# Kernel optimization log

Hardware: AMD Instinct MI355X
Metric: run time of the kernel (lower is better)

The kernel has to match this reference:

```python
import jax, jax.numpy as jnp
import numpy as np

N = 10000
E = 160000
B = 16
NEG_SLOPE = 0.2


def gat_conv(x, src, dst, W, a_src, a_dst, b, heads, ch):
    # x: [N, F_in]; src/dst: [E'] (self-loops included); W: [F_in, heads*ch]
    n = x.shape[0]
    h = (x @ W).reshape(n, heads, ch)                     # [N,H,C]
    alpha_src = jnp.sum(h * a_src, axis=-1)               # [N,H]
    alpha_dst = jnp.sum(h * a_dst, axis=-1)               # [N,H]
    e = jax.nn.leaky_relu(alpha_src[src] + alpha_dst[dst], NEG_SLOPE)  # [E,H]
    # segment softmax over edges grouped by destination node
    m = jax.ops.segment_max(e, dst, num_segments=n)       # [N,H]
    ex = jnp.exp(e - m[dst])                              # [E,H]
    denom = jax.ops.segment_sum(ex, dst, num_segments=n)  # [N,H]
    alpha = ex / denom[dst]                               # [E,H]
    out = jax.ops.segment_sum(alpha[:, :, None] * h[src], dst, num_segments=n)  # [N,H,C]
    return out.reshape(n, heads * ch) + b


def setup_inputs() -> dict:
    key = jax.random.key(0)
    ks = jax.random.split(key, 16)
    glorot = lambda k, shp: jax.random.normal(k, shp, jnp.float32) * np.sqrt(2.0 / (shp[0] + shp[-1]))
    inp = {
        "x": jax.random.normal(ks[0], (N, 128), jnp.float32),
        "edge_index": jax.random.randint(ks[1], (2, E), 0, N, jnp.int64),
        "batch": jnp.sort(jax.random.randint(ks[2], (N,), 0, B, jnp.int64)),
        # conv1: 128 -> 128 per head, 8 heads
        "W1": glorot(ks[3], (128, 8 * 128)),
        "att_src1": glorot(ks[4], (8, 128)),
        "att_dst1": glorot(ks[5], (8, 128)),
        "b1": jnp.zeros((8 * 128,), jnp.float32),
        # conv2: 1024 -> 64 per head, 8 heads
        "W2": glorot(ks[6], (1024, 8 * 64)),
        "att_src2": glorot(ks[7], (8, 64)),
        "att_dst2": glorot(ks[8], (8, 64)),
        "b2": jnp.zeros((8 * 64,), jnp.float32),
        "fc1_w": glorot(ks[9], (512, 32)),
        "fc1_b": jnp.zeros((32,), jnp.float32),
        "fc2_w": glorot(ks[10], (32, 10)),
        "fc2_b": jnp.zeros((10,), jnp.float32),
    }
    return inp


def reference(x, edge_index, batch, W1, att_src1, att_dst1, b1,
              W2, att_src2, att_dst2, b2, fc1_w, fc1_b, fc2_w, fc2_b):
    n = x.shape[0]
    loop = jnp.arange(n, dtype=edge_index.dtype)
    src = jnp.concatenate([edge_index[0], loop])  # PyG add_self_loops=True
    dst = jnp.concatenate([edge_index[1], loop])
    h = jax.nn.elu(gat_conv(x, src, dst, W1, att_src1, att_dst1, b1, 8, 128))   # [N,1024]
    h = jax.nn.elu(gat_conv(h, src, dst, W2, att_src2, att_dst2, b2, 8, 64))    # [N,512]
    # global mean pool over graphs
    sums = jax.ops.segment_sum(h, batch, num_segments=B)                        # [B,512]
    cnt = jax.ops.segment_sum(jnp.ones((n,), h.dtype), batch, num_segments=B)
    g = sums / jnp.maximum(cnt, 1.0)[:, None]
    g = jax.nn.elu(g @ fc1_w + fc1_b)
    return g @ fc2_w + fc2_b                                                    # [B,10]
```

## Files before the change

### kernel.cpp

```cpp
#include <hip/hip_runtime.h>
#include <math.h>

#define HEADS 8
#define NEG 0.2f

typedef unsigned short ushort_t;
typedef __attribute__((ext_vector_type(8))) short short8;
typedef float f32x4 __attribute__((ext_vector_type(4)));

__device__ inline ushort_t f2bf(float f) {
  union { float f; unsigned u; } v; v.f = f;
  unsigned r = (v.u + 0x7FFF + ((v.u >> 16) & 1)) >> 16;
  return (ushort_t)r;
}

__device__ inline float4 bf4(uint2 v) {
  union { unsigned u; float f; } a, b, c, d;
  a.u = v.x << 16; b.u = v.x & 0xffff0000u;
  c.u = v.y << 16; d.u = v.y & 0xffff0000u;
  return make_float4(a.f, b.f, c.f, d.f);
}

__global__ void zero_k(int* __restrict__ p, int n) {
  int i = blockIdx.x * blockDim.x + threadIdx.x;
  int stride = gridDim.x * blockDim.x;
  for (; i < n; i += stride) p[i] = 0;
}

__global__ void prep_k(const int* __restrict__ ei, int* __restrict__ src,
                       int* __restrict__ dst, int* __restrict__ deg, int E, int Nn) {
  int i = blockIdx.x * blockDim.x + threadIdx.x;
  if (i >= E + Nn) return;
  int s, d;
  if (i < E) { s = ei[i]; d = ei[E + i]; }
  else       { s = d = i - E; }
  src[i] = s;
  dst[i] = d;
  atomicAdd(&deg[d], 1);
}

__global__ __launch_bounds__(1024) void scan_k(const int* __restrict__ deg,
                                               int* __restrict__ offs,
                                               int* __restrict__ cursor, int Nn) {
  __shared__ int wtot[16];
  __shared__ int wexcl[16];
  __shared__ int soff_s;
  int t = threadIdx.x;
  int lane = t & 63, w = t >> 6;
  if (t == 0) soff_s = 0;
  __syncthreads();
  for (int base = 0; base < Nn; base += 4096) {
    int idx = base + 4 * t;
    int4 v = make_int4(0, 0, 0, 0);
    if (idx + 3 < Nn) v = *(const int4*)&deg[idx];
    else {
      if (idx < Nn)     v.x = deg[idx];
      if (idx + 1 < Nn) v.y = deg[idx + 1];
      if (idx + 2 < Nn) v.z = deg[idx + 2];
      if (idx + 3 < Nn) v.w = deg[idx + 3];
    }
    int s1 = v.x, s2 = s1 + v.y, s3 = s2 + v.z, s4 = s3 + v.w;
    int sc = s4;
#pragma unroll
    for (int o = 1; o < 64; o <<= 1) {
      int x = __shfl_up(sc, o);
      if (lane >= o) sc += x;
    }
    if (lane == 63) wtot[w] = sc;
    __syncthreads();
    if (w == 0) {
      int tv = (lane < 16) ? wtot[lane] : 0;
      int ts = tv;
#pragma unroll
      for (int o = 1; o < 16; o <<= 1) {
        int x = __shfl_up(ts, o);
        if (lane >= o) ts += x;
      }
      if (lane < 16) wexcl[lane] = ts - tv;
      if (lane == 15) wtot[15] = ts;
    }
    __syncthreads();
    int excl = soff_s + wexcl[w] + (sc - s4);
    int o0 = excl, o1 = excl + s1, o2 = excl + s2, o3 = excl + s3;
    if (idx < Nn)     { offs[idx] = o0;     cursor[idx] = o0; }
    if (idx + 1 < Nn) { offs[idx + 1] = o1; cursor[idx + 1] = o1; }
    if (idx + 2 < Nn) { offs[idx + 2] = o2; cursor[idx + 2] = o2; }
    if (idx + 3 < Nn) { offs[idx + 3] = o3; cursor[idx + 3] = o3; }
    int chunk_total = wtot[15];
    __syncthreads();
    if (t == 0) soff_s += chunk_total;
    __syncthreads();
  }
  if (t == 0) offs[Nn] = soff_s;
}

__global__ void scatter_k(const int* __restrict__ src, const int* __restrict__ dst,
                          int* __restrict__ cursor, int* __restrict__ psrc, int Etot) {
  int i = blockIdx.x * blockDim.x + threadIdx.x;
  if (i >= Etot) return;
  int p = atomicAdd(&cursor[dst[i]], 1);
  psrc[p] = src[i];
}

__global__ void cast_k(const float* __restrict__ in, ushort_t* __restrict__ out, int n4) {
  int i = blockIdx.x * blockDim.x + threadIdx.x;
  if (i >= n4) return;
  float4 v = ((const float4*)in)[i];
  ushort_t o[4] = {f2bf(v.x), f2bf(v.y), f2bf(v.z), f2bf(v.w)};
  *(uint2*)&out[i * 4] = *(uint2*)o;
}

__global__ void tcast_k(const float* __restrict__ W, ushort_t* __restrict__ Wt, int K, int N) {
  int idx = blockIdx.x * blockDim.x + threadIdx.x;
  if (idx >= K * N) return;
  int n = idx / K, k = idx - n * K;
  Wt[idx] = f2bf(W[(size_t)k * N + n]);
}

#define LDA 40
__global__ __launch_bounds__(256) void mfma_gemm_k(const ushort_t* __restrict__ A,
                                                   const ushort_t* __restrict__ Bt,
                                                   ushort_t* __restrict__ Cb,
                                                   const float* __restrict__ att_s,
                                                   const float* __restrict__ att_d,
                                                   float* __restrict__ asrc,
                                                   float* __restrict__ adst,
                                                   int M, int N, int K, int CSHIFT) {
  __shared__ ushort_t As[128 * LDA];
  __shared__ ushort_t Bs[128 * LDA];
  int tid = threadIdx.x;
  int lane = tid & 63;
  int wave = tid >> 6;
  int wm = (wave >> 1) * 64, wn = (wave & 1) * 64;
  int bm = blockIdx.y * 128, bn = blockIdx.x * 128;
  int lrow = lane & 15, lq = lane >> 4;

  f32x4 acc[4][4];
#pragma unroll
  for (int i = 0; i < 4; i++)
#pragma unroll
    for (int j = 0; j < 4; j++) acc[i][j] = 0.f;

  int srow = tid >> 2;
  int skc = (tid & 3) * 8;

  for (int k0 = 0; k0 < K; k0 += 32) {
    int gr0 = min(bm + srow, M - 1);
    int gr1 = min(bm + srow + 64, M - 1);
    short8 va0 = *(const short8*)&A[(size_t)gr0 * K + k0 + skc];
    short8 va1 = *(const short8*)&A[(size_t)gr1 * K + k0 + skc];
    short8 vb0 = *(const short8*)&Bt[(size_t)(bn + srow) * K + k0 + skc];
    short8 vb1 = *(const short8*)&Bt[(size_t)(bn + srow + 64) * K + k0 + skc];
    __syncthreads();
    *(short8*)&As[srow * LDA + skc] = va0;
    *(short8*)&As[(srow + 64) * LDA + skc] = va1;
    *(short8*)&Bs[srow * LDA + skc] = vb0;
    *(short8*)&Bs[(srow + 64) * LDA + skc] = vb1;
    __syncthreads();
    short8 af[4], bfr[4];
#pragma unroll
    for (int t = 0; t < 4; t++) {
      af[t]  = *(const short8*)&As[(wm + t * 16 + lrow) * LDA + lq * 8];
      bfr[t] = *(const short8*)&Bs[(wn + t * 16 + lrow) * LDA + lq * 8];
    }
#pragma unroll
    for (int i = 0; i < 4; i++)
#pragma unroll
      for (int j = 0; j < 4; j++)
        acc[i][j] = __builtin_amdgcn_mfma_f32_16x16x32_bf16(af[i], bfr[j], acc[i][j], 0, 0, 0);
  }

  {
    int hh = (bn + wn) >> CSHIFT;
    float avs[4], avd[4];
#pragma unroll
    for (int j = 0; j < 4; j++) {
      int col = bn + wn + j * 16 + lrow;
      avs[j] = att_s[col];
      avd[j] = att_d[col];
    }
#pragma unroll
    for (int i = 0; i < 4; i++) {
#pragma unroll
      for (int r = 0; r < 4; r++) {
        float ps = 0.f, pd = 0.f;
#pragma unroll
        for (int j = 0; j < 4; j++) {
          float v = acc[i][j][r];
          ps += v * avs[j];
          pd += v * avd[j];
        }
#pragma unroll
        for (int o = 1; o < 16; o <<= 1) {
          ps += __shfl_xor(ps, o);
          pd += __shfl_xor(pd, o);
        }
        int row = bm + wm + i * 16 + lq * 4 + r;
        if (lrow == 0 && row < M) {
          atomicAdd(&asrc[row * HEADS + hh], ps);
          atomicAdd(&adst[row * HEADS + hh], pd);
        }
      }
    }
  }

#pragma unroll
  for (int i = 0; i < 4; i++) {
    int row0 = bm + wm + i * 16 + lq * 4;
#pragma unroll
    for (int j = 0; j < 4; j++) {
      int col = bn + wn + j * 16 + lrow;
#pragma unroll
      for (int r = 0; r < 4; r++) {
        int row = row0 + r;
        if (row < M) Cb[(size_t)row * N + col] = f2bf(acc[i][j][r]);
      }
    }
  }
}

template <int F, int CSHIFT, int BT, typename OT>
__global__ __launch_bounds__(BT) void aggregate_k(const ushort_t* __restrict__ hb,
                                                  const float* __restrict__ asrc,
                                                  const float* __restrict__ adst,
                                                  const int* __restrict__ offs,
                                                  const int* __restrict__ psrc,
                                                  const float* __restrict__ bias,
                                                  OT* __restrict__ out) {
  constexpr int CH = 128;
  __shared__ int ls[CH];
  __shared__ float lw[CH][HEADS];
  __shared__ float adn[HEADS];
  int n = blockIdx.x;
  int t = threadIdx.x;
  int c0 = 4 * t;
  int hh = c0 >> CSHIFT;
  if (t < HEADS) adn[t] = adst[n * HEADS + t];
  float4 acc = make_float4(0.f, 0.f, 0.f, 0.f);
  float wsum = 0.f;
  int e0 = offs[n], deg = offs[n + 1] - e0;
  for (int base = 0; base < deg; base += CH) {
    int m = min(CH, deg - base);
    __syncthreads();
    if (t < m) ls[t] = psrc[e0 + base + t];
    __syncthreads();
    for (int idx = t; idx < m * HEADS; idx += BT) {
      int e = idx >> 3, h = idx & 7;
      float v = asrc[ls[e] * HEADS + h] + adn[h];
      v = (v > 0.f) ? v : NEG * v;
      lw[e][h] = expf(v);
    }
    __syncthreads();
    int i = 0;
    for (; i + 8 <= m; i += 8) {
      int s[8];
      uint2 r[8];
      float w[8];
#pragma unroll
      for (int u = 0; u < 8; u++) s[u] = ls[i + u];
#pragma unroll
      for (int u = 0; u < 8; u++) r[u] = *(const uint2*)&hb[(size_t)s[u] * F + c0];
#pragma unroll
      for (int u = 0; u < 8; u++) w[u] = lw[i + u][hh];
#pragma unroll
      for (int u = 0; u < 8; u++) {
        float4 f = bf4(r[u]);
        wsum += w[u];
        acc.x += w[u] * f.x;
        acc.y += w[u] * f.y;
        acc.z += w[u] * f.z;
        acc.w += w[u] * f.w;
      }
    }
    for (; i < m; i++) {
      int s0 = ls[i];
      float w0 = lw[i][hh];
      float4 f0 = bf4(*(const uint2*)&hb[(size_t)s0 * F + c0]);
      wsum += w0;
      acc.x += w0 * f0.x; acc.y += w0 * f0.y;
      acc.z += w0 * f0.z; acc.w += w0 * f0.w;
    }
  }
  float inv = 1.f / wsum;
  float v0 = acc.x * inv + bias[c0];
  float v1 = acc.y * inv + bias[c0 + 1];
  float v2 = acc.z * inv + bias[c0 + 2];
  float v3 = acc.w * inv + bias[c0 + 3];
  v0 = (v0 > 0.f) ? v0 : expm1f(v0);
  v1 = (v1 > 0.f) ? v1 : expm1f(v1);
  v2 = (v2 > 0.f) ? v2 : expm1f(v2);
  v3 = (v3 > 0.f) ? v3 : expm1f(v3);
  if (sizeof(OT) == 2) {
    unsigned p0 = (unsigned)f2bf(v0) | ((unsigned)f2bf(v1) << 16);
    unsigned p1 = (unsigned)f2bf(v2) | ((unsigned)f2bf(v3) << 16);
    *(uint2*)&((ushort_t*)out)[(size_t)n * F + c0] = make_uint2(p0, p1);
  } else {
    *(float4*)&((float*)out)[(size_t)n * F + c0] = make_float4(v0, v1, v2, v3);
  }
}

__global__ void bounds_k(const int* __restrict__ batch, int* __restrict__ bstart,
                         int* __restrict__ bend, int Nn) {
  int i = blockIdx.x * blockDim.x + threadIdx.x;
  if (i >= Nn) return;
  int b = batch[i];
  if (i == 0 || batch[i - 1] != b) bstart[b] = i;
  if (i == Nn - 1 || batch[i + 1] != b) bend[b] = i + 1;
}

__global__ __launch_bounds__(256) void pool_k(const float* __restrict__ g,
                                              const int* __restrict__ batch,
                                              float* __restrict__ sums, int Nn) {
  int c = blockIdx.x * 256 + threadIdx.x;
  int n0 = blockIdx.y * 50;
  int n1 = min(n0 + 50, Nn);
  if (n0 >= n1) return;
  float acc = 0.f;
  int cur = batch[n0];
  for (int n = n0; n < n1; n++) {
    int b = batch[n];
    if (b != cur) { atomicAdd(&sums[cur * 512 + c], acc); acc = 0.f; cur = b; }
    acc += g[(size_t)n * 512 + c];
  }
  atomicAdd(&sums[cur * 512 + c], acc);
}

__global__ __launch_bounds__(512) void mlp_k(const float* __restrict__ sums,
                                             const int* __restrict__ bstart,
                                             const int* __restrict__ bend,
                                             const float* __restrict__ w1,
                                             const float* __restrict__ b1,
                                             const float* __restrict__ w2,
                                             const float* __restrict__ b2,
                                             float* __restrict__ out) {
  __shared__ float gm[16 * 512];
  __shared__ float t1[16 * 32];
  int t = threadIdx.x;
  for (int i = t; i < 16 * 512; i += 512) {
    int b = i >> 9;
    float c = (float)(bend[b] - bstart[b]);
    gm[i] = sums[i] / fmaxf(c, 1.f);
  }
  __syncthreads();
  {
    int b = t >> 5, j = t & 31;
    float s = b1[j];
    for (int k = 0; k < 512; k++) s += gm[(b << 9) + k] * w1[k * 32 + j];
    t1[t] = (s > 0.f) ? s : expm1f(s);
  }
  __syncthreads();
  if (t < 160) {
    int b = t / 10, j = t - b * 10;
    float s = b2[j];
#pragma unroll
    for (int k = 0; k < 32; k++) s += t1[b * 32 + k] * w2[k * 10 + j];
    out[t] = s;
  }
}

extern "C" void kernel_launch(void* const* d_in, const int* in_sizes, int n_in,
                              void* d_out, int out_size, void* d_ws, size_t ws_size,
                              hipStream_t stream) {
  const float* x   = (const float*)d_in[0];
  const int*   ei  = (const int*)d_in[1];
  const int* batch = (const int*)d_in[2];
  const float* W1  = (const float*)d_in[3];
  const float* as1 = (const float*)d_in[4];
  const float* ad1 = (const float*)d_in[5];
  const float* b1  = (const float*)d_in[6];
  const float* W2  = (const float*)d_in[7];
  const float* as2 = (const float*)d_in[8];
  const float* ad2 = (const float*)d_in[9];
  const float* b2  = (const float*)d_in[10];
  const float* f1w = (const float*)d_in[11];
  const float* f1b = (const float*)d_in[12];
  const float* f2w = (const float*)d_in[13];
  const float* f2b = (const float*)d_in[14];
  float* out = (float*)d_out;

  const int Nn = in_sizes[2];
  const int E = in_sizes[1] / 2;
  const int Etot = E + Nn;

  size_t off = 0;
  auto alloc = [&](size_t elems) { size_t o = off; off += (elems + 63) & ~(size_t)63; return o; };
  int* wsi = (int*)d_ws;
  float* wsf = (float*)d_ws;

  size_t o_deg  = alloc(Nn);
  size_t o_pool = alloc(16 * 512);
  size_t o_bst  = alloc(64);
  size_t o_ben  = alloc(64);
  size_t o_as1  = alloc((size_t)Nn * 8);
  size_t o_ad1  = alloc((size_t)Nn * 8);
  size_t o_as2  = alloc((size_t)Nn * 8);
  size_t o_ad2  = alloc((size_t)Nn * 8);
  size_t zero_words = off;
  size_t o_offs = alloc(Nn + 1);
  size_t o_cur  = alloc(Nn);
  size_t o_src  = alloc(Etot);
  size_t o_dst  = alloc(Etot);
  size_t o_psrc = alloc(Etot);
  size_t o_xb   = alloc((size_t)Nn * 128 / 2);
  size_t o_w1t  = alloc(1024 * 128 / 2);
  size_t o_w2t  = alloc(512 * 1024 / 2);
  size_t o_h    = alloc((size_t)Nn * 1024 / 2);
  size_t o_g    = alloc((size_t)Nn * 1024);

  ushort_t* xb  = (ushort_t*)(wsi + o_xb);
  ushort_t* w1t = (ushort_t*)(wsi + o_w1t);
  ushort_t* w2t = (ushort_t*)(wsi + o_w2t);
  ushort_t* hb  = (ushort_t*)(wsi + o_h);
  ushort_t* g1b = (ushort_t*)(wsi + o_g);

  int eb = (Etot + 255) / 256;

  zero_k<<<512, 256, 0, stream>>>(wsi, (int)zero_words);
  prep_k<<<eb, 256, 0, stream>>>(ei, wsi + o_src, wsi + o_dst, wsi + o_deg, E, Nn);
  scan_k<<<1, 1024, 0, stream>>>(wsi + o_deg, wsi + o_offs, wsi + o_cur, Nn);
  scatter_k<<<eb, 256, 0, stream>>>(wsi + o_src, wsi + o_dst, wsi + o_cur,
                                    wsi + o_psrc, Etot);

  cast_k<<<(Nn * 128 / 4 + 255) / 256, 256, 0, stream>>>(x, xb, Nn * 128 / 4);
  tcast_k<<<(128 * 1024 + 255) / 256, 256, 0, stream>>>(W1, w1t, 128, 1024);
  tcast_k<<<(1024 * 512 + 255) / 256, 256, 0, stream>>>(W2, w2t, 1024, 512);

  mfma_gemm_k<<<dim3(1024 / 128, (Nn + 127) / 128), 256, 0, stream>>>(
      xb, w1t, hb, as1, ad1, wsf + o_as1, wsf + o_ad1, Nn, 1024, 128, 7);
  aggregate_k<1024, 7, 256, ushort_t><<<Nn, 256, 0, stream>>>(
      hb, wsf + o_as1, wsf + o_ad1, wsi + o_offs, wsi + o_psrc, b1, g1b);

  mfma_gemm_k<<<dim3(512 / 128, (Nn + 127) / 128), 256, 0, stream>>>(
      g1b, w2t, hb, as2, ad2, wsf + o_as2, wsf + o_ad2, Nn, 512, 1024, 6);
  aggregate_k<512, 6, 128, float><<<Nn, 128, 0, stream>>>(
      hb, wsf + o_as2, wsf + o_ad2, wsi + o_offs, wsi + o_psrc, b2, wsf + o_g);

  bounds_k<<<(Nn + 255) / 256, 256, 0, stream>>>(batch, wsi + o_bst, wsi + o_ben, Nn);
  pool_k<<<dim3(2, (Nn + 49) / 50), 256, 0, stream>>>(wsf + o_g, batch, wsf + o_pool, Nn);
  mlp_k<<<1, 512, 0, stream>>>(wsf + o_pool, wsi + o_bst, wsi + o_ben, f1w, f1b, f2w, f2b, out);
}
```

Baseline: 308.7 us.

## Drop LDS staging in GAT aggregation, split channels across blocks, prefetch indices

```diff
diff --git a/kernel.cpp b/kernel.cpp
--- a/kernel.cpp
+++ b/kernel.cpp
@@ -219,7 +219,7 @@
   }
 }
 
-template <int F, int CSHIFT, int BT, typename OT>
+template <int F, int CSHIFT, int BT, int NSPLIT, typename OT>
 __global__ __launch_bounds__(BT) void aggregate_k(const ushort_t* __restrict__ hb,
                                                   const float* __restrict__ asrc,
                                                   const float* __restrict__ adst,
@@ -227,60 +227,63 @@
                                                   const int* __restrict__ psrc,
                                                   const float* __restrict__ bias,
                                                   OT* __restrict__ out) {
-  constexpr int CH = 128;
-  __shared__ int ls[CH];
-  __shared__ float lw[CH][HEADS];
-  __shared__ float adn[HEADS];
-  int n = blockIdx.x;
+  constexpr int CPB = F / NSPLIT;
+  static_assert(CPB == 4 * BT, "CPB/thread mismatch");
+  int nb = blockIdx.x;
+  int n = nb / NSPLIT;
+  int coff = (nb - n * NSPLIT) * CPB;
   int t = threadIdx.x;
-  int c0 = 4 * t;
+  int c0 = coff + 4 * t;
   int hh = c0 >> CSHIFT;
-  if (t < HEADS) adn[t] = adst[n * HEADS + t];
+  float adn = adst[n * HEADS + hh];
+  int e0 = offs[n], e1 = offs[n + 1];
   float4 acc = make_float4(0.f, 0.f, 0.f, 0.f);
   float wsum = 0.f;
-  int e0 = offs[n], deg = offs[n + 1] - e0;
-  for (int base = 0; base < deg; base += CH) {
-    int m = min(CH, deg - base);
-    __syncthreads();
-    if (t < m) ls[t] = psrc[e0 + base + t];
-    __syncthreads();
-    for (int idx = t; idx < m * HEADS; idx += BT) {
-      int e = idx >> 3, h = idx & 7;
-      float v = asrc[ls[e] * HEADS + h] + adn[h];
+
+  int i = e0;
+  int s[8];
+  if (i + 8 <= e1) {
+#pragma unroll
+    for (int u = 0; u < 8; u++) s[u] = psrc[i + u];
+  }
+  while (i + 8 <= e1) {
+    uint2 r[8];
+    float av[8];
+#pragma unroll
+    for (int u = 0; u < 8; u++) r[u] = *(const uint2*)&hb[(size_t)s[u] * F + c0];
+#pragma unroll
+    for (int u = 0; u < 8; u++) av[u] = asrc[s[u] * HEADS + hh];
+    i += 8;
+    bool more = (i + 8 <= e1);
+    int sn[8];
+#pragma unroll
+    for (int u = 0; u < 8; u++) sn[u] = more ? psrc[i + u] : 0;
+#pragma unroll
+    for (int u = 0; u < 8; u++) {
+      float v = av[u] + adn;
       v = (v > 0.f) ? v : NEG * v;
-      lw[e][h] = expf(v);
-    }
-    __syncthreads();
-    int i = 0;
-    for (; i + 8 <= m; i += 8) {
-      int s[8];
-      uint2 r[8];
-      float w[8];
-#pragma unroll
-      for (int u = 0; u < 8; u++) s[u] = ls[i + u];
-#pragma unroll
-      for (int u = 0; u < 8; u++) r[u] = *(const uint2*)&hb[(size_t)s[u] * F + c0];
-#pragma unroll
-      for (int u = 0; u < 8; u++) w[u] = lw[i + u][hh];
-#pragma unroll
-      for (int u = 0; u < 8; u++) {
-        float4 f = bf4(r[u]);
-        wsum += w[u];
-        acc.x += w[u] * f.x;
-        acc.y += w[u] * f.y;
-        acc.z += w[u] * f.z;
-        acc.w += w[u] * f.w;
-      }
-    }
-    for (; i < m; i++) {
-      int s0 = ls[i];
-      float w0 = lw[i][hh];
-      float4 f0 = bf4(*(const uint2*)&hb[(size_t)s0 * F + c0]);
-      wsum += w0;
-      acc.x += w0 * f0.x; acc.y += w0 * f0.y;
-      acc.z += w0 * f0.z; acc.w += w0 * f0.w;
-    }
-  }
+      float w = expf(v);
+      float4 f = bf4(r[u]);
+      wsum += w;
+      acc.x += w * f.x;
+      acc.y += w * f.y;
+      acc.z += w * f.z;
+      acc.w += w * f.w;
+    }
+#pragma unroll
+    for (int u = 0; u < 8; u++) s[u] = sn[u];
+  }
+  for (; i < e1; i++) {
+    int ss = psrc[i];
+    float v = asrc[ss * HEADS + hh] + adn;
+    v = (v > 0.f) ? v : NEG * v;
+    float w = expf(v);
+    float4 f = bf4(*(const uint2*)&hb[(size_t)ss * F + c0]);
+    wsum += w;
+    acc.x += w * f.x; acc.y += w * f.y;
+    acc.z += w * f.z; acc.w += w * f.w;
+  }
+
   float inv = 1.f / wsum;
   float v0 = acc.x * inv + bias[c0];
   float v1 = acc.y * inv + bias[c0 + 1];
@@ -427,12 +430,12 @@
 
   mfma_gemm_k<<<dim3(1024 / 128, (Nn + 127) / 128), 256, 0, stream>>>(
       xb, w1t, hb, as1, ad1, wsf + o_as1, wsf + o_ad1, Nn, 1024, 128, 7);
-  aggregate_k<1024, 7, 256, ushort_t><<<Nn, 256, 0, stream>>>(
+  aggregate_k<1024, 7, 128, 2, ushort_t><<<Nn * 2, 128, 0, stream>>>(
       hb, wsf + o_as1, wsf + o_ad1, wsi + o_offs, wsi + o_psrc, b1, g1b);
 
   mfma_gemm_k<<<dim3(512 / 128, (Nn + 127) / 128), 256, 0, stream>>>(
       g1b, w2t, hb, as2, ad2, wsf + o_as2, wsf + o_ad2, Nn, 512, 1024, 6);
-  aggregate_k<512, 6, 128, float><<<Nn, 128, 0, stream>>>(
+  aggregate_k<512, 6, 64, 2, float><<<Nn * 2, 64, 0, stream>>>(
       hb, wsf + o_as2, wsf + o_ad2, wsi + o_offs, wsi + o_psrc, b2, wsf + o_g);
 
   bounds_k<<<(Nn + 255) / 256, 256, 0, stream>>>(batch, wsi + o_bst, wsi + o_ben, Nn);
```

Result: faster. 297.4 us (-3.7%).
